# Optimization experiments

Measured on AMD Instinct MI355X. Metric: run time of the kernel, lower is better.

## Reference

```python
import math
import jax, jax.numpy as jnp
from jax import lax
import numpy as np

THETA = 10.0      # spiking threshold
TAU_SR = 10.0     # SRM (psp) alpha-kernel time constant
TAU_REF = 1.0     # refractory alpha-kernel time constant
SCALE_REF = 2.0   # refractory scale (kernel = -scaleRef*theta*alpha)
TAU_RHO = 1.0     # surrogate-gradient width
TS = 1.0          # simulation time step


def _alpha_filter_scan(x, tau, extra_input_fn=None):
    """Causal convolution along last (time) axis with alpha kernel
    k[n] = (n*Ts/tau) * exp(1 - n*Ts/tau)  (k[0] = 0),
    implemented exactly as a 2-state linear recurrence.
    x: [N, C, T] -> out: [N, C, T]."""
    d = jnp.float32(math.exp(-TS / tau))
    c = jnp.float32(math.e * TS / tau)
    xT = jnp.moveaxis(x, -1, 0)  # [T, N, C]

    def step(carry, xt):
        p, a = carry
        a = d * (a + p)          # alpha response from inputs up to t-1
        p = d * p + xt           # pure exponential state
        return (p, a), a * c

    z = jnp.zeros_like(xT[0])
    _, out = lax.scan(step, (z, z), xT)
    return jnp.moveaxis(out, 0, -1)


def psp(x):
    return _alpha_filter_scan(x, TAU_SR)


@jax.custom_vjp
def spike_fn(v):
    # Heaviside threshold on (membrane - theta)
    return (v >= 0).astype(v.dtype)

def _spike_fwd(v):
    return spike_fn(v), v

def _spike_bwd(v, g):
    # SLAYER surrogate gradient: exponential pdf around threshold
    grad = (1.0 / TAU_RHO) * jnp.exp(-jnp.abs(v) / TAU_RHO)
    return (g * grad,)

spike_fn.defvjp(_spike_fwd, _spike_bwd)


def spike_layer(u_in):
    """Threshold-and-refract over time. u_in: [N, C, T] psp potentials.
    Refractory response = -scaleRef*theta * alpha_{tauRef}(past spikes)."""
    d = jnp.float32(math.exp(-TS / TAU_REF))
    c = jnp.float32(math.e * TS / TAU_REF)
    ref_scale = jnp.float32(-SCALE_REF * THETA)
    uT = jnp.moveaxis(u_in, -1, 0)  # [T, N, C]

    def step(carry, ut):
        p, a = carry
        a = d * (a + p)                      # refractory potential at t
        u = ut + c * a                       # membrane potential
        s = spike_fn(u - THETA)              # spikes (0/1)
        p = d * p + ref_scale * s            # inject refractory impulse
        return (p, a), s

    z = jnp.zeros_like(uT[0])
    _, s = lax.scan(step, (z, z), uT)
    return jnp.moveaxis(s, 0, -1)


def setup_inputs() -> dict:
    key = jax.random.key(0)
    k1, k2, k3 = jax.random.split(key, 3)
    N, I, H, O, T = 64, 256, 1024, 18, 500
    # Bernoulli(0.1) input spikes
    spike_input = (jax.random.uniform(k1, (N, I, T)) < 0.1).astype(jnp.float32)
    W1 = jax.random.normal(k2, (H, I), dtype=jnp.float32) * (1.0 / math.sqrt(I))
    W2 = jax.random.normal(k3, (O, H), dtype=jnp.float32) * (1.0 / math.sqrt(H))
    return {"spike_input": spike_input, "W1": W1, "W2": W2}


def reference(spike_input, W1, W2):
    # layer 1: dense (per-timestep linear) -> psp -> spike
    y1 = jnp.einsum('nit,hi->nht', spike_input, W1)
    s1 = spike_layer(psp(y1))
    # layer 2
    y2 = jnp.einsum('nht,oh->not', s1, W2)
    s2 = spike_layer(psp(y2))
    return s2
```

## Files before the change

kernel.cpp:

```cpp
#include <hip/hip_runtime.h>


#define NN 64
#define II 256
#define HH 1024
#define OO 18
#define TT 500

#define D_SR 0.9048374180359595f
#define C_SR 0.27182818284590454f
#define D_RF 0.36787944117144233f
#define C_RF 2.718281828459045f
#define THETA 10.0f
#define REFS (-20.0f)

typedef _Float16 f16;
typedef _Float16 f16x8 __attribute__((ext_vector_type(8)));
typedef float f32x4 __attribute__((ext_vector_type(4)));
typedef unsigned int uint;
typedef unsigned long long u64;

__device__ __forceinline__ void gl2lds16(const void* g, void* l) {
    __builtin_amdgcn_global_load_lds(
        (const __attribute__((address_space(1))) void*)g,
        (__attribute__((address_space(3))) void*)l, 16, 0, 0);
}

__launch_bounds__(256)
__global__ void prep_all(const float* __restrict__ X, const float* __restrict__ W1,
                         const float* __restrict__ W2, f16* __restrict__ Xb,
                         f16* __restrict__ W1h, f16* __restrict__ W1l,
                         f16* __restrict__ W2h, f16* __restrict__ W2l) {
    __shared__ float tile[64][65];
    const int b = blockIdx.x;
    const int tid = threadIdx.x;

    if (b < 2048) {
        const int t0 = (b & 7) * 64, i0 = ((b >> 3) & 3) * 64, n = b >> 5;
        const int tx = tid & 63, q = tid >> 6;
        const float* Xn = X + (size_t)n * II * TT;
#pragma unroll 4
        for (int j = 0; j < 16; ++j) {
            int il = j * 4 + q;
            int t = t0 + tx;
            tile[il][tx] = (t < TT) ? Xn[(size_t)(i0 + il) * TT + t] : 0.f;
        }
        __syncthreads();
#pragma unroll 4
        for (int j = 0; j < 16; ++j) {
            int tl = j * 4 + q;
            int t = t0 + tl;
            if (t < TT)
                Xb[((size_t)n * TT + t) * II + i0 + tx] = (f16)tile[tx][tl];
        }
    } else if (b < 3072) {
        int idx = (b - 2048) * 256 + tid;
        float w = W1[idx];
        f16 h = (f16)w;
        f16 l = (f16)(w - (float)h);
        W1h[idx] = h;
        W1l[idx] = l;
    } else {
        int idx = (b - 3072) * 256 + tid;
        int o = idx >> 10;
        float w = (o < OO) ? W2[idx] : 0.f;
        f16 h = (f16)w;
        f16 l = (f16)(w - (float)h);
        W2h[idx] = h;
        W2l[idx] = l;
    }
}

__launch_bounds__(512)
__global__ void gemm1_scan1(const f16* __restrict__ Xb, const f16* __restrict__ Wh,
                            const f16* __restrict__ Wl, u64* __restrict__ Sb) {
    __shared__ __align__(16) char smem[3 * 24576];
    float* yb = (float*)smem;

    const int tid = threadIdx.x;
    const int wave = tid >> 6, lane = tid & 63;

    const int f = blockIdx.y * 8 + blockIdx.x;
    const int x = f & 7, g = f >> 3;
    const int n = x * 8 + (g & 7);
    const int ht = g >> 3;
    const int h0g = ht * 128;

    const int rbl = wave * 16 + (lane >> 2);
    const int koff = (((lane & 3) ^ ((lane >> 3) & 3))) * 8;
    const f16* gBh0 = Wh + (size_t)(h0g + rbl) * II + koff;
    const f16* gBl0 = Wl + (size_t)(h0g + rbl) * II + koff;

    const int wm = wave & 1, wn = wave >> 1;
    const int fr = lane & 15, kq = lane >> 4;
    const int kz = (kq ^ ((fr >> 1) & 3)) * 8;

    float p1 = 0.f, a1 = 0.f, p2 = 0.f, a2 = 0.f;

    for (int c = 0; c < 4; ++c) {
        const int t0 = c * 128;
        const int TCe = (TT - t0 < 128) ? (TT - t0) : 128;

        int r0 = rbl; if (r0 > TCe - 1) r0 = TCe - 1;
        const f16* gA0 = Xb + ((size_t)n * TT + t0 + r0) * II + koff;

        auto stage = [&](int kk2, int b) {
            f16* As_b = (f16*)(smem + b * 24576);
            f16* Bh_b = As_b + 4096;
            f16* Bl_b = As_b + 8192;
            const int ko = kk2 * 32;
            gl2lds16(gA0 + ko, As_b + wave * 512);
            gl2lds16(gBh0 + ko, Bh_b + wave * 512);
            gl2lds16(gBl0 + ko, Bl_b + wave * 512);
        };

        stage(0, 0);
        stage(1, 1);

        f32x4 acc[4][2] = {};
#pragma unroll
        for (int kk = 0; kk < 8; ++kk) {
            if (kk < 7) asm volatile("s_waitcnt vmcnt(3)" ::: "memory");
            else        asm volatile("s_waitcnt vmcnt(0)" ::: "memory");
            __builtin_amdgcn_s_barrier();
            __builtin_amdgcn_sched_barrier(0);
            if (kk < 6) stage(kk + 2, (kk + 2) % 3);

            const f16* As_b = (const f16*)(smem + (kk % 3) * 24576);
            const f16* Bh_b = As_b + 4096;
            const f16* Bl_b = As_b + 8192;

            f16x8 av[4], bhv[2], blv[2];
#pragma unroll
            for (int i = 0; i < 4; ++i)
                av[i] = *(const f16x8*)(As_b + (wm * 64 + i * 16 + fr) * 32 + kz);
#pragma unroll
            for (int j = 0; j < 2; ++j) {
                bhv[j] = *(const f16x8*)(Bh_b + (wn * 32 + j * 16 + fr) * 32 + kz);
                blv[j] = *(const f16x8*)(Bl_b + (wn * 32 + j * 16 + fr) * 32 + kz);
            }
            __builtin_amdgcn_s_setprio(1);
#pragma unroll
            for (int i = 0; i < 4; ++i)
#pragma unroll
                for (int j = 0; j < 2; ++j) {
                    acc[i][j] = __builtin_amdgcn_mfma_f32_16x16x32_f16(av[i], bhv[j], acc[i][j], 0, 0, 0);
                    acc[i][j] = __builtin_amdgcn_mfma_f32_16x16x32_f16(av[i], blv[j], acc[i][j], 0, 0, 0);
                }
            __builtin_amdgcn_s_setprio(0);
        }
        __syncthreads();

#pragma unroll
        for (int i = 0; i < 4; ++i)
#pragma unroll
            for (int j = 0; j < 2; ++j) {
                int tr = wm * 64 + i * 16 + kq * 4;
                int hc = wn * 32 + j * 16 + fr;
#pragma unroll
                for (int r = 0; r < 4; ++r)
                    yb[(tr + r) * 132 + hc] = acc[i][j][r];
            }
        __syncthreads();

        if (tid < 128) {
            u64* sq = Sb + ((size_t)n * TT + t0) * 16 + ht * 2 + wave;
            float rb_[8];
#pragma unroll
            for (int j = 0; j < 8; ++j) rb_[j] = yb[j * 132 + tid];
            int t = 0;
            for (; t + 8 <= TCe; t += 8) {
#pragma unroll
                for (int j = 0; j < 8; ++j) {
                    float xv = rb_[j];
                    int tn = t + j + 8;
                    rb_[j] = (tn < TCe) ? yb[tn * 132 + tid] : 0.f;
                    a1 = D_SR * (a1 + p1);
                    p1 = D_SR * p1 + xv;
                    float ut = C_SR * a1;
                    a2 = D_RF * (a2 + p2);
                    float u = ut + C_RF * a2;
                    float s = (u >= THETA) ? 1.0f : 0.0f;
                    p2 = D_RF * p2 + REFS * s;
                    u64 m = __ballot(u >= THETA);
                    if (lane == 0) sq[(size_t)(t + j) * 16] = m;
                }
            }
            int rem = TCe - t;
#pragma unroll
            for (int j = 0; j < 8; ++j) {
                if (j < rem) {
                    float xv = rb_[j];
                    a1 = D_SR * (a1 + p1);
                    p1 = D_SR * p1 + xv;
                    float ut = C_SR * a1;
                    a2 = D_RF * (a2 + p2);
                    float u = ut + C_RF * a2;
                    float s = (u >= THETA) ? 1.0f : 0.0f;
                    p2 = D_RF * p2 + REFS * s;
                    u64 m = __ballot(u >= THETA);
                    if (lane == 0) sq[(size_t)(t + j) * 16] = m;
                }
            }
        }
        __syncthreads();
    }
}

__launch_bounds__(256)
__global__ void gemm2_mfma(const uint* __restrict__ Ab, const f16* __restrict__ W2h,
                           const f16* __restrict__ W2l, float* __restrict__ Y2) {
    __shared__ __align__(16) char bsm[4][3][4096];

    const int tid = threadIdx.x;
    const int wave = tid >> 6, lane = tid & 63;
    const int m0 = blockIdx.x * 64;
    const int fr = lane & 15, kq = lane >> 4;

    const int row = m0 + wave * 16 + fr;
    const uint* arow = Ab + (size_t)row * 32;
    const int sh = kq * 8;
    uint wrow[32];
#pragma unroll
    for (int q = 0; q < 8; ++q)
        *(uint4*)&wrow[q * 4] = *(const uint4*)(arow + q * 4);

    const int srow = lane >> 2;
    const int koff = (((lane & 3) ^ ((lane >> 3) & 3))) * 8;
    const f16* gh0 = W2h + (size_t)srow * HH + koff;
    const f16* gh1 = W2h + (size_t)(srow + 16) * HH + koff;
    const f16* gl0 = W2l + (size_t)srow * HH + koff;
    const f16* gl1 = W2l + (size_t)(srow + 16) * HH + koff;

    auto stage = [&](int kk2, int b) {
        char* s = bsm[wave][b];
        const int ko = kk2 * 32;
        gl2lds16(gh0 + ko, s);
        gl2lds16(gh1 + ko, s + 1024);
        gl2lds16(gl0 + ko, s + 2048);
        gl2lds16(gl1 + ko, s + 3072);
    };

    stage(0, 0);
    stage(1, 1);

    const int kz = (kq ^ ((fr >> 1) & 3)) * 8;

    f32x4 acc[2] = {};
#pragma unroll
    for (int kk = 0; kk < HH / 32; ++kk) {
        if (kk < HH / 32 - 1) asm volatile("s_waitcnt vmcnt(4)" ::: "memory");
        else                  asm volatile("s_waitcnt vmcnt(0)" ::: "memory");
        __builtin_amdgcn_sched_barrier(0);
        if (kk < HH / 32 - 2) stage(kk + 2, (kk + 2) % 3);

        const f16* Bh_b = (const f16*)bsm[wave][kk % 3];
        const f16* Bl_b = Bh_b + 2048 / 2;

        const uint byte = (wrow[kk] >> sh) & 0xFFu;
        f16x8 a;
#pragma unroll
        for (int e = 0; e < 8; ++e)
            a[e] = (byte & (1u << e)) ? (f16)1.0f : (f16)0.0f;

        f16x8 bh[2], bl[2];
#pragma unroll
        for (int j = 0; j < 2; ++j) {
            bh[j] = *(const f16x8*)(Bh_b + (j * 16 + fr) * 32 + kz);
            bl[j] = *(const f16x8*)(Bl_b + (j * 16 + fr) * 32 + kz);
        }
#pragma unroll
        for (int j = 0; j < 2; ++j) {
            acc[j] = __builtin_amdgcn_mfma_f32_16x16x32_f16(a, bh[j], acc[j], 0, 0, 0);
            acc[j] = __builtin_amdgcn_mfma_f32_16x16x32_f16(a, bl[j], acc[j], 0, 0, 0);
        }
    }

#pragma unroll
    for (int j = 0; j < 2; ++j) {
        int rbase = m0 + wave * 16 + kq * 4;
        int cc = j * 16 + fr;
        float* p = Y2 + (size_t)rbase * 32 + cc;
#pragma unroll
        for (int r = 0; r < 4; ++r)
            p[(size_t)r * 32] = acc[j][r];
    }
}

__launch_bounds__(256)
__global__ void scan2_k(const float* __restrict__ Y2, float* __restrict__ Out) {
    __shared__ float yc[TT * 32];
    __shared__ float sb[OO * TT];
    const int n = blockIdx.x, tid = threadIdx.x;

    const float4* src = (const float4*)(Y2 + (size_t)n * TT * 32);
    float4* dst = (float4*)yc;
    for (int i = tid; i < TT * 8; i += 256) dst[i] = src[i];
    __syncthreads();

    if (tid < 32) {
        float p1 = 0.f, a1 = 0.f, p2 = 0.f, a2 = 0.f;
        float rb_[8];
#pragma unroll
        for (int j = 0; j < 8; ++j) rb_[j] = yc[j * 32 + tid];
        int t = 0;
        for (; t + 8 <= TT; t += 8) {
#pragma unroll
            for (int j = 0; j < 8; ++j) {
                float xv = rb_[j];
                int tn = t + j + 8;
                rb_[j] = (tn < TT) ? yc[tn * 32 + tid] : 0.f;
                a1 = D_SR * (a1 + p1);
                p1 = D_SR * p1 + xv;
                float ut = C_SR * a1;
                a2 = D_RF * (a2 + p2);
                float u = ut + C_RF * a2;
                float s = (u >= THETA) ? 1.0f : 0.0f;
                p2 = D_RF * p2 + REFS * s;
                if (tid < OO) sb[tid * TT + t + j] = s;
            }
        }
#pragma unroll
        for (int j = 0; j < 8; ++j) {
            if (t + j < TT) {
                float xv = rb_[j];
                a1 = D_SR * (a1 + p1);
                p1 = D_SR * p1 + xv;
                float ut = C_SR * a1;
                a2 = D_RF * (a2 + p2);
                float u = ut + C_RF * a2;
                float s = (u >= THETA) ? 1.0f : 0.0f;
                p2 = D_RF * p2 + REFS * s;
                if (tid < OO) sb[tid * TT + t + j] = s;
            }
        }
    }
    __syncthreads();

    float* on = Out + (size_t)n * OO * TT;
    for (int e = tid; e < OO * TT; e += 256) on[e] = sb[e];
}

extern "C" void kernel_launch(void* const* d_in, const int* in_sizes, int n_in,
                              void* d_out, int out_size, void* d_ws, size_t ws_size,
                              hipStream_t stream) {
    const float* X  = (const float*)d_in[0];
    const float* W1 = (const float*)d_in[1];
    const float* W2 = (const float*)d_in[2];
    float* out = (float*)d_out;

    const size_t s_sb = (size_t)NN * TT * 16 * 8;
    const size_t s_Xb = (size_t)NN * TT * II * 2;
    const size_t s_W  = (size_t)HH * II * 2;
    const size_t s_W2 = (size_t)32 * HH * 2;

    char* w = (char*)d_ws;
    u64*   sbb = (u64*)w;  w += s_sb;
    f16*   Xb  = (f16*)w;  w += s_Xb;
    f16*   W1h = (f16*)w;  w += s_W;
    f16*   W1l = (f16*)w;  w += s_W;
    f16*   W2h = (f16*)w;  w += s_W2;
    f16*   W2l = (f16*)w;  w += s_W2;
    float* y2  = (float*)w;

    prep_all<<<3200, 256, 0, stream>>>(X, W1, W2, Xb, W1h, W1l, W2h, W2l);

    gemm1_scan1<<<dim3(8, NN), 512, 0, stream>>>(Xb, W1h, W1l, sbb);

    gemm2_mfma<<<(NN * TT) / 64, 256, 0, stream>>>((const uint*)sbb, W2h, W2l, y2);
    scan2_k<<<NN, 256, 0, stream>>>(y2, out);
}
```

Baseline: 189.1 us.

## Bit-pack input spikes and fuse layer-2 GEMM with output scan

Input spikes are packed into 1-bit ballot masks in prep instead of fp16, and gemm1 expands them in registers, so the A tile no longer goes through LDS. The layer-2 GEMM and second scan are merged into one kernel per batch element, with the GEMM output kept in shared memory instead of a global Y2 buffer. Each wave in the fused kernel now computes 64 time rows. This cuts global traffic and one launch, but leaves only 64 blocks for the layer-2 GEMM and needs a large LDS allocation.

```diff
diff --git a/kernel.cpp b/kernel.cpp
--- a/kernel.cpp
+++ b/kernel.cpp
@@ -6,6 +6,7 @@
 #define HH 1024
 #define OO 18
 #define TT 500
+#define TTP 512
 
 #define D_SR 0.9048374180359595f
 #define C_SR 0.27182818284590454f
@@ -26,9 +27,19 @@
         (__attribute__((address_space(3))) void*)l, 16, 0, 0);
 }
 
+__device__ __forceinline__ f16x8 expand8(uint by) {
+    union { f16x8 v; uint u[4]; } A;
+#pragma unroll
+    for (int e = 0; e < 4; ++e) {
+        uint b0 = (by >> (2 * e)) & 1u, b1 = (by >> (2 * e + 1)) & 1u;
+        A.u[e] = (b0 ? 0x3C00u : 0u) | (b1 ? 0x3C000000u : 0u);
+    }
+    return A.v;
+}
+
 __launch_bounds__(256)
 __global__ void prep_all(const float* __restrict__ X, const float* __restrict__ W1,
-                         const float* __restrict__ W2, f16* __restrict__ Xb,
+                         const float* __restrict__ W2, u64* __restrict__ Xb,
                          f16* __restrict__ W1h, f16* __restrict__ W1l,
                          f16* __restrict__ W2h, f16* __restrict__ W2l) {
     __shared__ float tile[64][65];
@@ -46,12 +57,14 @@
             tile[il][tx] = (t < TT) ? Xn[(size_t)(i0 + il) * TT + t] : 0.f;
         }
         __syncthreads();
-#pragma unroll 4
-        for (int j = 0; j < 16; ++j) {
-            int tl = j * 4 + q;
-            int t = t0 + tl;
-            if (t < TT)
-                Xb[((size_t)n * TT + t) * II + i0 + tx] = (f16)tile[tx][tl];
+        const int wv = tid >> 6, ln = tid & 63;
+        const int widx = (b >> 3) & 3;
+#pragma unroll
+        for (int tt = 0; tt < 16; ++tt) {
+            int t = wv * 16 + tt;
+            u64 m = __ballot(tile[ln][t] != 0.0f);
+            if (ln == 0 && (t0 + t) < TT)
+                Xb[((size_t)n * TTP + t0 + t) * 4 + widx] = m;
         }
     } else if (b < 3072) {
         int idx = (b - 2048) * 256 + tid;
@@ -71,10 +84,10 @@
     }
 }
 
-__launch_bounds__(512)
-__global__ void gemm1_scan1(const f16* __restrict__ Xb, const f16* __restrict__ Wh,
+__launch_bounds__(512, 4)
+__global__ void gemm1_scan1(const uint* __restrict__ Xb32, const f16* __restrict__ Wh,
                             const f16* __restrict__ Wl, u64* __restrict__ Sb) {
-    __shared__ __align__(16) char smem[3 * 24576];
+    __shared__ __align__(16) char smem[67584];
     float* yb = (float*)smem;
 
     const int tid = threadIdx.x;
@@ -94,6 +107,7 @@
     const int wm = wave & 1, wn = wave >> 1;
     const int fr = lane & 15, kq = lane >> 4;
     const int kz = (kq ^ ((fr >> 1) & 3)) * 8;
+    const int sh = kq * 8;
 
     float p1 = 0.f, a1 = 0.f, p2 = 0.f, a2 = 0.f;
 
@@ -101,39 +115,45 @@
         const int t0 = c * 128;
         const int TCe = (TT - t0 < 128) ? (TT - t0) : 128;
 
-        int r0 = rbl; if (r0 > TCe - 1) r0 = TCe - 1;
-        const f16* gA0 = Xb + ((size_t)n * TT + t0 + r0) * II + koff;
+        uint xb[8];
+#pragma unroll
+        for (int i = 0; i < 4; ++i) {
+            int r = t0 + wm * 64 + i * 16 + fr;
+            if (r > TT - 1) r = TT - 1;
+            const uint* xr = Xb32 + ((size_t)n * TTP + r) * 8;
+            uint4 wA = *(const uint4*)xr;
+            uint4 wB = *(const uint4*)(xr + 4);
+            xb[i * 2 + 0] = ((wA.x >> sh) & 0xFFu) | (((wA.y >> sh) & 0xFFu) << 8)
+                          | (((wA.z >> sh) & 0xFFu) << 16) | (((wA.w >> sh) & 0xFFu) << 24);
+            xb[i * 2 + 1] = ((wB.x >> sh) & 0xFFu) | (((wB.y >> sh) & 0xFFu) << 8)
+                          | (((wB.z >> sh) & 0xFFu) << 16) | (((wB.w >> sh) & 0xFFu) << 24);
+        }
 
         auto stage = [&](int kk2, int b) {
-            f16* As_b = (f16*)(smem + b * 24576);
-            f16* Bh_b = As_b + 4096;
-            f16* Bl_b = As_b + 8192;
+            f16* Bh_b = (f16*)(smem + b * 16384);
             const int ko = kk2 * 32;
-            gl2lds16(gA0 + ko, As_b + wave * 512);
             gl2lds16(gBh0 + ko, Bh_b + wave * 512);
-            gl2lds16(gBl0 + ko, Bl_b + wave * 512);
+            gl2lds16(gBl0 + ko, Bh_b + 4096 + wave * 512);
         };
-
         stage(0, 0);
         stage(1, 1);
 
         f32x4 acc[4][2] = {};
 #pragma unroll
         for (int kk = 0; kk < 8; ++kk) {
-            if (kk < 7) asm volatile("s_waitcnt vmcnt(3)" ::: "memory");
+            if (kk < 7) asm volatile("s_waitcnt vmcnt(2)" ::: "memory");
             else        asm volatile("s_waitcnt vmcnt(0)" ::: "memory");
             __builtin_amdgcn_s_barrier();
             __builtin_amdgcn_sched_barrier(0);
             if (kk < 6) stage(kk + 2, (kk + 2) % 3);
 
-            const f16* As_b = (const f16*)(smem + (kk % 3) * 24576);
-            const f16* Bh_b = As_b + 4096;
-            const f16* Bl_b = As_b + 8192;
+            const f16* Bh_b = (const f16*)(smem + (kk % 3) * 16384);
+            const f16* Bl_b = Bh_b + 4096;
 
             f16x8 av[4], bhv[2], blv[2];
 #pragma unroll
             for (int i = 0; i < 4; ++i)
-                av[i] = *(const f16x8*)(As_b + (wm * 64 + i * 16 + fr) * 32 + kz);
+                av[i] = expand8((xb[i * 2 + (kk >> 2)] >> ((kk & 3) * 8)) & 0xFFu);
 #pragma unroll
             for (int j = 0; j < 2; ++j) {
                 bhv[j] = *(const f16x8*)(Bh_b + (wn * 32 + j * 16 + fr) * 32 + kz);
@@ -207,33 +227,28 @@
     }
 }
 
-__launch_bounds__(256)
-__global__ void gemm2_mfma(const uint* __restrict__ Ab, const f16* __restrict__ W2h,
-                           const f16* __restrict__ W2l, float* __restrict__ Y2) {
-    __shared__ __align__(16) char bsm[4][3][4096];
-
-    const int tid = threadIdx.x;
+__launch_bounds__(512)
+__global__ void gemm2_scan2(const uint* __restrict__ Ab, const f16* __restrict__ W2h,
+                            const f16* __restrict__ W2l, float* __restrict__ Out) {
+    __shared__ __align__(16) char L[162304];
+    float* yc = (float*)(L + 98304);
+    float* sb = (float*)L;
+
+    const int n = blockIdx.x, tid = threadIdx.x;
     const int wave = tid >> 6, lane = tid & 63;
-    const int m0 = blockIdx.x * 64;
     const int fr = lane & 15, kq = lane >> 4;
-
-    const int row = m0 + wave * 16 + fr;
-    const uint* arow = Ab + (size_t)row * 32;
     const int sh = kq * 8;
-    uint wrow[32];
-#pragma unroll
-    for (int q = 0; q < 8; ++q)
-        *(uint4*)&wrow[q * 4] = *(const uint4*)(arow + q * 4);
-
     const int srow = lane >> 2;
     const int koff = (((lane & 3) ^ ((lane >> 3) & 3))) * 8;
+    const int kz = (kq ^ ((fr >> 1) & 3)) * 8;
+
     const f16* gh0 = W2h + (size_t)srow * HH + koff;
     const f16* gh1 = W2h + (size_t)(srow + 16) * HH + koff;
     const f16* gl0 = W2l + (size_t)srow * HH + koff;
     const f16* gl1 = W2l + (size_t)(srow + 16) * HH + koff;
 
     auto stage = [&](int kk2, int b) {
-        char* s = bsm[wave][b];
+        char* s = L + (wave * 3 + b) * 4096;
         const int ko = kk2 * 32;
         gl2lds16(gh0 + ko, s);
         gl2lds16(gh1 + ko, s + 1024);
@@ -241,27 +256,34 @@
         gl2lds16(gl1 + ko, s + 3072);
     };
 
+    const uint* ar[4];
+#pragma unroll
+    for (int mi = 0; mi < 4; ++mi) {
+        int t = wave * 64 + mi * 16 + fr;
+        if (t > TT - 1) t = TT - 1;
+        ar[mi] = Ab + (size_t)(n * TT + t) * 32;
+    }
+
+    uint ac[4], an[4];
+#pragma unroll
+    for (int mi = 0; mi < 4; ++mi) ac[mi] = ar[mi][0];
     stage(0, 0);
     stage(1, 1);
 
-    const int kz = (kq ^ ((fr >> 1) & 3)) * 8;
-
-    f32x4 acc[2] = {};
-#pragma unroll
-    for (int kk = 0; kk < HH / 32; ++kk) {
-        if (kk < HH / 32 - 1) asm volatile("s_waitcnt vmcnt(4)" ::: "memory");
-        else                  asm volatile("s_waitcnt vmcnt(0)" ::: "memory");
+    f32x4 acc[4][2] = {};
+#pragma unroll
+    for (int kk = 0; kk < 32; ++kk) {
+        if (kk < 31) asm volatile("s_waitcnt vmcnt(4)" ::: "memory");
+        else         asm volatile("s_waitcnt vmcnt(0)" ::: "memory");
         __builtin_amdgcn_sched_barrier(0);
-        if (kk < HH / 32 - 2) stage(kk + 2, (kk + 2) % 3);
-
-        const f16* Bh_b = (const f16*)bsm[wave][kk % 3];
-        const f16* Bl_b = Bh_b + 2048 / 2;
-
-        const uint byte = (wrow[kk] >> sh) & 0xFFu;
-        f16x8 a;
-#pragma unroll
-        for (int e = 0; e < 8; ++e)
-            a[e] = (byte & (1u << e)) ? (f16)1.0f : (f16)0.0f;
+        if (kk < 31) {
+#pragma unroll
+            for (int mi = 0; mi < 4; ++mi) an[mi] = ar[mi][kk + 1];
+        }
+        if (kk < 30) stage(kk + 2, (kk + 2) % 3);
+
+        const f16* Bh_b = (const f16*)(L + (wave * 3 + kk % 3) * 4096);
+        const f16* Bl_b = Bh_b + 1024;
 
         f16x8 bh[2], bl[2];
 #pragma unroll
@@ -269,33 +291,31 @@
             bh[j] = *(const f16x8*)(Bh_b + (j * 16 + fr) * 32 + kz);
             bl[j] = *(const f16x8*)(Bl_b + (j * 16 + fr) * 32 + kz);
         }
+        __builtin_amdgcn_s_setprio(1);
+#pragma unroll
+        for (int mi = 0; mi < 4; ++mi) {
+            f16x8 a = expand8((ac[mi] >> sh) & 0xFFu);
+#pragma unroll
+            for (int j = 0; j < 2; ++j) {
+                acc[mi][j] = __builtin_amdgcn_mfma_f32_16x16x32_f16(a, bh[j], acc[mi][j], 0, 0, 0);
+                acc[mi][j] = __builtin_amdgcn_mfma_f32_16x16x32_f16(a, bl[j], acc[mi][j], 0, 0, 0);
+            }
+        }
+        __builtin_amdgcn_s_setprio(0);
+#pragma unroll
+        for (int mi = 0; mi < 4; ++mi) ac[mi] = an[mi];
+    }
+
+#pragma unroll
+    for (int mi = 0; mi < 4; ++mi)
 #pragma unroll
         for (int j = 0; j < 2; ++j) {
-            acc[j] = __builtin_amdgcn_mfma_f32_16x16x32_f16(a, bh[j], acc[j], 0, 0, 0);
-            acc[j] = __builtin_amdgcn_mfma_f32_16x16x32_f16(a, bl[j], acc[j], 0, 0, 0);
-        }
-    }
-
-#pragma unroll
-    for (int j = 0; j < 2; ++j) {
-        int rbase = m0 + wave * 16 + kq * 4;
-        int cc = j * 16 + fr;
-        float* p = Y2 + (size_t)rbase * 32 + cc;
-#pragma unroll
-        for (int r = 0; r < 4; ++r)
-            p[(size_t)r * 32] = acc[j][r];
-    }
-}
-
-__launch_bounds__(256)
-__global__ void scan2_k(const float* __restrict__ Y2, float* __restrict__ Out) {
-    __shared__ float yc[TT * 32];
-    __shared__ float sb[OO * TT];
-    const int n = blockIdx.x, tid = threadIdx.x;
-
-    const float4* src = (const float4*)(Y2 + (size_t)n * TT * 32);
-    float4* dst = (float4*)yc;
-    for (int i = tid; i < TT * 8; i += 256) dst[i] = src[i];
+            int tb = wave * 64 + mi * 16 + kq * 4;
+            int oc = j * 16 + fr;
+#pragma unroll
+            for (int r = 0; r < 4; ++r)
+                if (tb + r < TT) yc[(tb + r) * 32 + oc] = acc[mi][j][r];
+        }
     __syncthreads();
 
     if (tid < 32) {
@@ -338,7 +358,7 @@
     __syncthreads();
 
     float* on = Out + (size_t)n * OO * TT;
-    for (int e = tid; e < OO * TT; e += 256) on[e] = sb[e];
+    for (int e = tid; e < OO * TT; e += 512) on[e] = sb[e];
 }
 
 extern "C" void kernel_launch(void* const* d_in, const int* in_sizes, int n_in,
@@ -350,23 +370,21 @@
     float* out = (float*)d_out;
 
     const size_t s_sb = (size_t)NN * TT * 16 * 8;
-    const size_t s_Xb = (size_t)NN * TT * II * 2;
+    const size_t s_Xb = (size_t)NN * TTP * 32;
     const size_t s_W  = (size_t)HH * II * 2;
     const size_t s_W2 = (size_t)32 * HH * 2;
 
     char* w = (char*)d_ws;
     u64*   sbb = (u64*)w;  w += s_sb;
-    f16*   Xb  = (f16*)w;  w += s_Xb;
+    u64*   Xbt = (u64*)w;  w += s_Xb;
     f16*   W1h = (f16*)w;  w += s_W;
     f16*   W1l = (f16*)w;  w += s_W;
     f16*   W2h = (f16*)w;  w += s_W2;
     f16*   W2l = (f16*)w;  w += s_W2;
-    float* y2  = (float*)w;
-
-    prep_all<<<3200, 256, 0, stream>>>(X, W1, W2, Xb, W1h, W1l, W2h, W2l);
-
-    gemm1_scan1<<<dim3(8, NN), 512, 0, stream>>>(Xb, W1h, W1l, sbb);
-
-    gemm2_mfma<<<(NN * TT) / 64, 256, 0, stream>>>((const uint*)sbb, W2h, W2l, y2);
-    scan2_k<<<NN, 256, 0, stream>>>(y2, out);
-}
+
+    prep_all<<<3200, 256, 0, stream>>>(X, W1, W2, Xbt, W1h, W1l, W2h, W2l);
+
+    gemm1_scan1<<<dim3(8, NN), 512, 0, stream>>>((const uint*)Xbt, W1h, W1l, sbb);
+
+    gemm2_scan2<<<NN, 512, 0, stream>>>((const uint*)sbb, W2h, W2l, out);
+}
```

Result: slower. 226.5 us (+19.8%).

## Fuse gemm1/scan1, gemm2 and scan2 into one persistent kernel with flag sync

Applied to the files above, without the earlier changes.

Merges the three post-prep kernels into a single 512-block kernel. Each block does its layer-1 GEMM and scan tile, then signals per-sample completion counters. Blocks then spin on those counters before running the layer-2 GEMM, and the first 64 blocks spin again before running the final scan, which now writes straight to global memory. This removes launch gaps and lets stages overlap across samples. It relies on all 512 blocks being co-resident to avoid deadlock, and the spin-waits and atomics add overhead.

```diff
diff --git a/kernel.cpp b/kernel.cpp
--- a/kernel.cpp
+++ b/kernel.cpp
@@ -30,7 +30,8 @@
 __global__ void prep_all(const float* __restrict__ X, const float* __restrict__ W1,
                          const float* __restrict__ W2, f16* __restrict__ Xb,
                          f16* __restrict__ W1h, f16* __restrict__ W1l,
-                         f16* __restrict__ W2h, f16* __restrict__ W2l) {
+                         f16* __restrict__ W2h, f16* __restrict__ W2l,
+                         uint* __restrict__ flags) {
     __shared__ float tile[64][65];
     const int b = blockIdx.x;
     const int tid = threadIdx.x;
@@ -61,6 +62,7 @@
         W1h[idx] = h;
         W1l[idx] = l;
     } else {
+        if (b == 3072 && tid < 128) flags[tid] = 0;
         int idx = (b - 3072) * 256 + tid;
         int o = idx >> 10;
         float w = (o < OO) ? W2[idx] : 0.f;
@@ -71,110 +73,269 @@
     }
 }
 
-__launch_bounds__(512)
-__global__ void gemm1_scan1(const f16* __restrict__ Xb, const f16* __restrict__ Wh,
-                            const f16* __restrict__ Wl, u64* __restrict__ Sb) {
+__launch_bounds__(512, 4)
+__global__ void mega(const f16* __restrict__ Xb, const f16* __restrict__ Wh,
+                     const f16* __restrict__ Wl, u64* __restrict__ Sb,
+                     const f16* __restrict__ W2h, const f16* __restrict__ W2l,
+                     float* __restrict__ Y2, float* __restrict__ Out,
+                     uint* __restrict__ flags) {
     __shared__ __align__(16) char smem[3 * 24576];
-    float* yb = (float*)smem;
-
+
+    const int b = blockIdx.x;
     const int tid = threadIdx.x;
     const int wave = tid >> 6, lane = tid & 63;
-
-    const int f = blockIdx.y * 8 + blockIdx.x;
-    const int x = f & 7, g = f >> 3;
-    const int n = x * 8 + (g & 7);
-    const int ht = g >> 3;
-    const int h0g = ht * 128;
-
-    const int rbl = wave * 16 + (lane >> 2);
-    const int koff = (((lane & 3) ^ ((lane >> 3) & 3))) * 8;
-    const f16* gBh0 = Wh + (size_t)(h0g + rbl) * II + koff;
-    const f16* gBl0 = Wl + (size_t)(h0g + rbl) * II + koff;
-
-    const int wm = wave & 1, wn = wave >> 1;
-    const int fr = lane & 15, kq = lane >> 4;
-    const int kz = (kq ^ ((fr >> 1) & 3)) * 8;
-
-    float p1 = 0.f, a1 = 0.f, p2 = 0.f, a2 = 0.f;
-
-    for (int c = 0; c < 4; ++c) {
-        const int t0 = c * 128;
-        const int TCe = (TT - t0 < 128) ? (TT - t0) : 128;
-
-        int r0 = rbl; if (r0 > TCe - 1) r0 = TCe - 1;
-        const f16* gA0 = Xb + ((size_t)n * TT + t0 + r0) * II + koff;
-
-        auto stage = [&](int kk2, int b) {
-            f16* As_b = (f16*)(smem + b * 24576);
-            f16* Bh_b = As_b + 4096;
-            f16* Bl_b = As_b + 8192;
+    uint* done = flags;
+    uint* y2f  = flags + 64;
+
+    {
+        float* yb = (float*)smem;
+        const int x = b & 7, g = b >> 3;
+        const int nA = x * 8 + (g & 7);
+        const int ht = g >> 3;
+        const int h0g = ht * 128;
+
+        const int rbl = wave * 16 + (lane >> 2);
+        const int koff = (((lane & 3) ^ ((lane >> 3) & 3))) * 8;
+        const f16* gBh0 = Wh + (size_t)(h0g + rbl) * II + koff;
+        const f16* gBl0 = Wl + (size_t)(h0g + rbl) * II + koff;
+
+        const int wm = wave & 1, wn = wave >> 1;
+        const int fr = lane & 15, kq = lane >> 4;
+        const int kz = (kq ^ ((fr >> 1) & 3)) * 8;
+
+        float p1 = 0.f, a1 = 0.f, p2 = 0.f, a2 = 0.f;
+
+        for (int c = 0; c < 4; ++c) {
+            const int t0 = c * 128;
+            const int TCe = (TT - t0 < 128) ? (TT - t0) : 128;
+
+            int r0 = rbl; if (r0 > TCe - 1) r0 = TCe - 1;
+            const f16* gA0 = Xb + ((size_t)nA * TT + t0 + r0) * II + koff;
+
+            auto stage = [&](int kk2, int bs) {
+                f16* As_b = (f16*)(smem + bs * 24576);
+                f16* Bh_b = As_b + 4096;
+                f16* Bl_b = As_b + 8192;
+                const int ko = kk2 * 32;
+                gl2lds16(gA0 + ko, As_b + wave * 512);
+                gl2lds16(gBh0 + ko, Bh_b + wave * 512);
+                gl2lds16(gBl0 + ko, Bl_b + wave * 512);
+            };
+            stage(0, 0);
+            stage(1, 1);
+
+            f32x4 acc[4][2] = {};
+#pragma unroll
+            for (int kk = 0; kk < 8; ++kk) {
+                if (kk < 7) asm volatile("s_waitcnt vmcnt(3)" ::: "memory");
+                else        asm volatile("s_waitcnt vmcnt(0)" ::: "memory");
+                __builtin_amdgcn_s_barrier();
+                __builtin_amdgcn_sched_barrier(0);
+                if (kk < 6) stage(kk + 2, (kk + 2) % 3);
+
+                const f16* As_b = (const f16*)(smem + (kk % 3) * 24576);
+                const f16* Bh_b = As_b + 4096;
+                const f16* Bl_b = As_b + 8192;
+
+                f16x8 av[4], bhv[2], blv[2];
+#pragma unroll
+                for (int i = 0; i < 4; ++i)
+                    av[i] = *(const f16x8*)(As_b + (wm * 64 + i * 16 + fr) * 32 + kz);
+#pragma unroll
+                for (int j = 0; j < 2; ++j) {
+                    bhv[j] = *(const f16x8*)(Bh_b + (wn * 32 + j * 16 + fr) * 32 + kz);
+                    blv[j] = *(const f16x8*)(Bl_b + (wn * 32 + j * 16 + fr) * 32 + kz);
+                }
+                __builtin_amdgcn_s_setprio(1);
+#pragma unroll
+                for (int i = 0; i < 4; ++i)
+#pragma unroll
+                    for (int j = 0; j < 2; ++j) {
+                        acc[i][j] = __builtin_amdgcn_mfma_f32_16x16x32_f16(av[i], bhv[j], acc[i][j], 0, 0, 0);
+                        acc[i][j] = __builtin_amdgcn_mfma_f32_16x16x32_f16(av[i], blv[j], acc[i][j], 0, 0, 0);
+                    }
+                __builtin_amdgcn_s_setprio(0);
+            }
+            __syncthreads();
+
+#pragma unroll
+            for (int i = 0; i < 4; ++i)
+#pragma unroll
+                for (int j = 0; j < 2; ++j) {
+                    int tr = wm * 64 + i * 16 + kq * 4;
+                    int hc = wn * 32 + j * 16 + fr;
+#pragma unroll
+                    for (int r = 0; r < 4; ++r)
+                        yb[(tr + r) * 132 + hc] = acc[i][j][r];
+                }
+            __syncthreads();
+
+            if (tid < 128) {
+                u64* sq = Sb + ((size_t)nA * TT + t0) * 16 + ht * 2 + wave;
+                float rb_[8];
+#pragma unroll
+                for (int j = 0; j < 8; ++j) rb_[j] = yb[j * 132 + tid];
+                int t = 0;
+                for (; t + 8 <= TCe; t += 8) {
+#pragma unroll
+                    for (int j = 0; j < 8; ++j) {
+                        float xv = rb_[j];
+                        int tn = t + j + 8;
+                        rb_[j] = (tn < TCe) ? yb[tn * 132 + tid] : 0.f;
+                        a1 = D_SR * (a1 + p1);
+                        p1 = D_SR * p1 + xv;
+                        float ut = C_SR * a1;
+                        a2 = D_RF * (a2 + p2);
+                        float u = ut + C_RF * a2;
+                        float s = (u >= THETA) ? 1.0f : 0.0f;
+                        p2 = D_RF * p2 + REFS * s;
+                        u64 m = __ballot(u >= THETA);
+                        if (lane == 0) sq[(size_t)(t + j) * 16] = m;
+                    }
+                }
+                int rem = TCe - t;
+#pragma unroll
+                for (int j = 0; j < 8; ++j) {
+                    if (j < rem) {
+                        float xv = rb_[j];
+                        a1 = D_SR * (a1 + p1);
+                        p1 = D_SR * p1 + xv;
+                        float ut = C_SR * a1;
+                        a2 = D_RF * (a2 + p2);
+                        float u = ut + C_RF * a2;
+                        float s = (u >= THETA) ? 1.0f : 0.0f;
+                        p2 = D_RF * p2 + REFS * s;
+                        u64 m = __ballot(u >= THETA);
+                        if (lane == 0) sq[(size_t)(t + j) * 16] = m;
+                    }
+                }
+            }
+            __syncthreads();
+        }
+
+        if (tid == 0) {
+            __threadfence();
+            __hip_atomic_fetch_add(done + nA, 1u, __ATOMIC_RELEASE, __HIP_MEMORY_SCOPE_AGENT);
+        }
+    }
+    __syncthreads();
+
+    const int n0 = (b * 64) / 500, n1 = (b * 64 + 63) / 500;
+    if (b < 500 && tid < 256) {
+        while (__hip_atomic_load(done + n0, __ATOMIC_ACQUIRE, __HIP_MEMORY_SCOPE_AGENT) < 8u)
+            __builtin_amdgcn_s_sleep(8);
+        if (n1 != n0)
+            while (__hip_atomic_load(done + n1, __ATOMIC_ACQUIRE, __HIP_MEMORY_SCOPE_AGENT) < 8u)
+                __builtin_amdgcn_s_sleep(8);
+
+        const uint* Ab = (const uint*)Sb;
+        const int m0 = b * 64;
+        const int fr = lane & 15, kq = lane >> 4;
+        const int sh = kq * 8;
+        const int srow = lane >> 2;
+        const int koff = (((lane & 3) ^ ((lane >> 3) & 3))) * 8;
+        const int kz = (kq ^ ((fr >> 1) & 3)) * 8;
+
+        const f16* gh0 = W2h + (size_t)srow * HH + koff;
+        const f16* gh1 = W2h + (size_t)(srow + 16) * HH + koff;
+        const f16* gl0 = W2l + (size_t)srow * HH + koff;
+        const f16* gl1 = W2l + (size_t)(srow + 16) * HH + koff;
+
+        auto stage2 = [&](int kk2, int bs) {
+            char* s = smem + (wave * 3 + bs) * 4096;
             const int ko = kk2 * 32;
-            gl2lds16(gA0 + ko, As_b + wave * 512);
-            gl2lds16(gBh0 + ko, Bh_b + wave * 512);
-            gl2lds16(gBl0 + ko, Bl_b + wave * 512);
+            gl2lds16(gh0 + ko, s);
+            gl2lds16(gh1 + ko, s + 1024);
+            gl2lds16(gl0 + ko, s + 2048);
+            gl2lds16(gl1 + ko, s + 3072);
         };
 
-        stage(0, 0);
-        stage(1, 1);
-
-        f32x4 acc[4][2] = {};
-#pragma unroll
-        for (int kk = 0; kk < 8; ++kk) {
-            if (kk < 7) asm volatile("s_waitcnt vmcnt(3)" ::: "memory");
-            else        asm volatile("s_waitcnt vmcnt(0)" ::: "memory");
-            __builtin_amdgcn_s_barrier();
+        const int row = m0 + wave * 16 + fr;
+        const uint* arow = Ab + (size_t)row * 32;
+
+        uint ac[1] = { arow[0] };
+        uint an;
+        stage2(0, 0);
+        stage2(1, 1);
+
+        f32x4 acc2[2] = {};
+#pragma unroll
+        for (int kk = 0; kk < 32; ++kk) {
+            if (kk < 31) asm volatile("s_waitcnt vmcnt(4)" ::: "memory");
+            else         asm volatile("s_waitcnt vmcnt(0)" ::: "memory");
             __builtin_amdgcn_sched_barrier(0);
-            if (kk < 6) stage(kk + 2, (kk + 2) % 3);
-
-            const f16* As_b = (const f16*)(smem + (kk % 3) * 24576);
-            const f16* Bh_b = As_b + 4096;
-            const f16* Bl_b = As_b + 8192;
-
-            f16x8 av[4], bhv[2], blv[2];
-#pragma unroll
-            for (int i = 0; i < 4; ++i)
-                av[i] = *(const f16x8*)(As_b + (wm * 64 + i * 16 + fr) * 32 + kz);
+            if (kk < 31) an = arow[kk + 1];
+            if (kk < 30) stage2(kk + 2, (kk + 2) % 3);
+
+            const f16* Bh_b = (const f16*)(smem + (wave * 3 + kk % 3) * 4096);
+            const f16* Bl_b = Bh_b + 1024;
+
+            const uint byte = (ac[0] >> sh) & 0xFFu;
+            union { f16x8 v; uint u[4]; } A;
+#pragma unroll
+            for (int e = 0; e < 4; ++e) {
+                uint b0 = (byte >> (2 * e)) & 1u, b1 = (byte >> (2 * e + 1)) & 1u;
+                A.u[e] = (b0 ? 0x3C00u : 0u) | (b1 ? 0x3C000000u : 0u);
+            }
+
+            f16x8 bh[2], bl[2];
 #pragma unroll
             for (int j = 0; j < 2; ++j) {
-                bhv[j] = *(const f16x8*)(Bh_b + (wn * 32 + j * 16 + fr) * 32 + kz);
-                blv[j] = *(const f16x8*)(Bl_b + (wn * 32 + j * 16 + fr) * 32 + kz);
-            }
-            __builtin_amdgcn_s_setprio(1);
-#pragma unroll
-            for (int i = 0; i < 4; ++i)
-#pragma unroll
-                for (int j = 0; j < 2; ++j) {
-                    acc[i][j] = __builtin_amdgcn_mfma_f32_16x16x32_f16(av[i], bhv[j], acc[i][j], 0, 0, 0);
-                    acc[i][j] = __builtin_amdgcn_mfma_f32_16x16x32_f16(av[i], blv[j], acc[i][j], 0, 0, 0);
-                }
-            __builtin_amdgcn_s_setprio(0);
-        }
+                bh[j] = *(const f16x8*)(Bh_b + (j * 16 + fr) * 32 + kz);
+                bl[j] = *(const f16x8*)(Bl_b + (j * 16 + fr) * 32 + kz);
+            }
+#pragma unroll
+            for (int j = 0; j < 2; ++j) {
+                acc2[j] = __builtin_amdgcn_mfma_f32_16x16x32_f16(A.v, bh[j], acc2[j], 0, 0, 0);
+                acc2[j] = __builtin_amdgcn_mfma_f32_16x16x32_f16(A.v, bl[j], acc2[j], 0, 0, 0);
+            }
+            ac[0] = an;
+        }
+
+#pragma unroll
+        for (int j = 0; j < 2; ++j) {
+            int rbase = m0 + wave * 16 + kq * 4;
+            int cc = j * 16 + fr;
+            float* p = Y2 + (size_t)rbase * 32 + cc;
+#pragma unroll
+            for (int r = 0; r < 4; ++r)
+                p[(size_t)r * 32] = acc2[j][r];
+        }
+    }
+    __syncthreads();
+    if (b < 500 && tid == 0) {
+        __threadfence();
+        __hip_atomic_fetch_add(y2f + n0, 1u, __ATOMIC_RELEASE, __HIP_MEMORY_SCOPE_AGENT);
+        if (n1 != n0)
+            __hip_atomic_fetch_add(y2f + n1, 1u, __ATOMIC_RELEASE, __HIP_MEMORY_SCOPE_AGENT);
+    }
+
+    if (b < 64) {
+        const int n = b;
+        const uint expn = (uint)(((n + 1) * 500 - 1) / 64 - (n * 500) / 64 + 1);
+        while (__hip_atomic_load(y2f + n, __ATOMIC_ACQUIRE, __HIP_MEMORY_SCOPE_AGENT) < expn)
+            __builtin_amdgcn_s_sleep(8);
         __syncthreads();
 
-#pragma unroll
-        for (int i = 0; i < 4; ++i)
-#pragma unroll
-            for (int j = 0; j < 2; ++j) {
-                int tr = wm * 64 + i * 16 + kq * 4;
-                int hc = wn * 32 + j * 16 + fr;
-#pragma unroll
-                for (int r = 0; r < 4; ++r)
-                    yb[(tr + r) * 132 + hc] = acc[i][j][r];
-            }
+        float* yc = (float*)smem;
+        const float4* src = (const float4*)(Y2 + (size_t)n * TT * 32);
+        float4* dst = (float4*)yc;
+        for (int i = tid; i < TT * 8; i += 512) dst[i] = src[i];
         __syncthreads();
 
-        if (tid < 128) {
-            u64* sq = Sb + ((size_t)n * TT + t0) * 16 + ht * 2 + wave;
+        if (tid < 32) {
+            float p1 = 0.f, a1 = 0.f, p2 = 0.f, a2 = 0.f;
             float rb_[8];
-#pragma unroll
-            for (int j = 0; j < 8; ++j) rb_[j] = yb[j * 132 + tid];
+            float* on = Out + (size_t)n * OO * TT + (size_t)tid * TT;
+#pragma unroll
+            for (int j = 0; j < 8; ++j) rb_[j] = yc[j * 32 + tid];
             int t = 0;
-            for (; t + 8 <= TCe; t += 8) {
+            for (; t + 8 <= TT; t += 8) {
 #pragma unroll
                 for (int j = 0; j < 8; ++j) {
                     float xv = rb_[j];
                     int tn = t + j + 8;
-                    rb_[j] = (tn < TCe) ? yb[tn * 132 + tid] : 0.f;
+                    rb_[j] = (tn < TT) ? yc[tn * 32 + tid] : 0.f;
                     a1 = D_SR * (a1 + p1);
                     p1 = D_SR * p1 + xv;
                     float ut = C_SR * a1;
@@ -182,14 +343,12 @@
                     float u = ut + C_RF * a2;
                     float s = (u >= THETA) ? 1.0f : 0.0f;
                     p2 = D_RF * p2 + REFS * s;
-                    u64 m = __ballot(u >= THETA);
-                    if (lane == 0) sq[(size_t)(t + j) * 16] = m;
-                }
-            }
-            int rem = TCe - t;
+                    if (tid < OO) on[t + j] = s;
+                }
+            }
 #pragma unroll
             for (int j = 0; j < 8; ++j) {
-                if (j < rem) {
+                if (t + j < TT) {
                     float xv = rb_[j];
                     a1 = D_SR * (a1 + p1);
                     p1 = D_SR * p1 + xv;
@@ -198,147 +357,11 @@
                     float u = ut + C_RF * a2;
                     float s = (u >= THETA) ? 1.0f : 0.0f;
                     p2 = D_RF * p2 + REFS * s;
-                    u64 m = __ballot(u >= THETA);
-                    if (lane == 0) sq[(size_t)(t + j) * 16] = m;
-                }
-            }
-        }
-        __syncthreads();
-    }
-}
-
-__launch_bounds__(256)
-__global__ void gemm2_mfma(const uint* __restrict__ Ab, const f16* __restrict__ W2h,
-                           const f16* __restrict__ W2l, float* __restrict__ Y2) {
-    __shared__ __align__(16) char bsm[4][3][4096];
-
-    const int tid = threadIdx.x;
-    const int wave = tid >> 6, lane = tid & 63;
-    const int m0 = blockIdx.x * 64;
-    const int fr = lane & 15, kq = lane >> 4;
-
-    const int row = m0 + wave * 16 + fr;
-    const uint* arow = Ab + (size_t)row * 32;
-    const int sh = kq * 8;
-    uint wrow[32];
-#pragma unroll
-    for (int q = 0; q < 8; ++q)
-        *(uint4*)&wrow[q * 4] = *(const uint4*)(arow + q * 4);
-
-    const int srow = lane >> 2;
-    const int koff = (((lane & 3) ^ ((lane >> 3) & 3))) * 8;
-    const f16* gh0 = W2h + (size_t)srow * HH + koff;
-    const f16* gh1 = W2h + (size_t)(srow + 16) * HH + koff;
-    const f16* gl0 = W2l + (size_t)srow * HH + koff;
-    const f16* gl1 = W2l + (size_t)(srow + 16) * HH + koff;
-
-    auto stage = [&](int kk2, int b) {
-        char* s = bsm[wave][b];
-        const int ko = kk2 * 32;
-        gl2lds16(gh0 + ko, s);
-        gl2lds16(gh1 + ko, s + 1024);
-        gl2lds16(gl0 + ko, s + 2048);
-        gl2lds16(gl1 + ko, s + 3072);
-    };
-
-    stage(0, 0);
-    stage(1, 1);
-
-    const int kz = (kq ^ ((fr >> 1) & 3)) * 8;
-
-    f32x4 acc[2] = {};
-#pragma unroll
-    for (int kk = 0; kk < HH / 32; ++kk) {
-        if (kk < HH / 32 - 1) asm volatile("s_waitcnt vmcnt(4)" ::: "memory");
-        else                  asm volatile("s_waitcnt vmcnt(0)" ::: "memory");
-        __builtin_amdgcn_sched_barrier(0);
-        if (kk < HH / 32 - 2) stage(kk + 2, (kk + 2) % 3);
-
-        const f16* Bh_b = (const f16*)bsm[wave][kk % 3];
-        const f16* Bl_b = Bh_b + 2048 / 2;
-
-        const uint byte = (wrow[kk] >> sh) & 0xFFu;
-        f16x8 a;
-#pragma unroll
-        for (int e = 0; e < 8; ++e)
-            a[e] = (byte & (1u << e)) ? (f16)1.0f : (f16)0.0f;
-
-        f16x8 bh[2], bl[2];
-#pragma unroll
-        for (int j = 0; j < 2; ++j) {
-            bh[j] = *(const f16x8*)(Bh_b + (j * 16 + fr) * 32 + kz);
-            bl[j] = *(const f16x8*)(Bl_b + (j * 16 + fr) * 32 + kz);
-        }
-#pragma unroll
-        for (int j = 0; j < 2; ++j) {
-            acc[j] = __builtin_amdgcn_mfma_f32_16x16x32_f16(a, bh[j], acc[j], 0, 0, 0);
-            acc[j] = __builtin_amdgcn_mfma_f32_16x16x32_f16(a, bl[j], acc[j], 0, 0, 0);
-        }
-    }
-
-#pragma unroll
-    for (int j = 0; j < 2; ++j) {
-        int rbase = m0 + wave * 16 + kq * 4;
-        int cc = j * 16 + fr;
-        float* p = Y2 + (size_t)rbase * 32 + cc;
-#pragma unroll
-        for (int r = 0; r < 4; ++r)
-            p[(size_t)r * 32] = acc[j][r];
-    }
-}
-
-__launch_bounds__(256)
-__global__ void scan2_k(const float* __restrict__ Y2, float* __restrict__ Out) {
-    __shared__ float yc[TT * 32];
-    __shared__ float sb[OO * TT];
-    const int n = blockIdx.x, tid = threadIdx.x;
-
-    const float4* src = (const float4*)(Y2 + (size_t)n * TT * 32);
-    float4* dst = (float4*)yc;
-    for (int i = tid; i < TT * 8; i += 256) dst[i] = src[i];
-    __syncthreads();
-
-    if (tid < 32) {
-        float p1 = 0.f, a1 = 0.f, p2 = 0.f, a2 = 0.f;
-        float rb_[8];
-#pragma unroll
-        for (int j = 0; j < 8; ++j) rb_[j] = yc[j * 32 + tid];
-        int t = 0;
-        for (; t + 8 <= TT; t += 8) {
-#pragma unroll
-            for (int j = 0; j < 8; ++j) {
-                float xv = rb_[j];
-                int tn = t + j + 8;
-                rb_[j] = (tn < TT) ? yc[tn * 32 + tid] : 0.f;
-                a1 = D_SR * (a1 + p1);
-                p1 = D_SR * p1 + xv;
-                float ut = C_SR * a1;
-                a2 = D_RF * (a2 + p2);
-                float u = ut + C_RF * a2;
-                float s = (u >= THETA) ? 1.0f : 0.0f;
-                p2 = D_RF * p2 + REFS * s;
-                if (tid < OO) sb[tid * TT + t + j] = s;
-            }
-        }
-#pragma unroll
-        for (int j = 0; j < 8; ++j) {
-            if (t + j < TT) {
-                float xv = rb_[j];
-                a1 = D_SR * (a1 + p1);
-                p1 = D_SR * p1 + xv;
-                float ut = C_SR * a1;
-                a2 = D_RF * (a2 + p2);
-                float u = ut + C_RF * a2;
-                float s = (u >= THETA) ? 1.0f : 0.0f;
-                p2 = D_RF * p2 + REFS * s;
-                if (tid < OO) sb[tid * TT + t + j] = s;
-            }
-        }
-    }
-    __syncthreads();
-
-    float* on = Out + (size_t)n * OO * TT;
-    for (int e = tid; e < OO * TT; e += 256) on[e] = sb[e];
+                    if (tid < OO) on[t + j] = s;
+                }
+            }
+        }
+    }
 }
 
 extern "C" void kernel_launch(void* const* d_in, const int* in_sizes, int n_in,
@@ -353,6 +376,7 @@
     const size_t s_Xb = (size_t)NN * TT * II * 2;
     const size_t s_W  = (size_t)HH * II * 2;
     const size_t s_W2 = (size_t)32 * HH * 2;
+    const size_t s_y2 = (size_t)NN * TT * 32 * 4;
 
     char* w = (char*)d_ws;
     u64*   sbb = (u64*)w;  w += s_sb;
@@ -361,12 +385,10 @@
     f16*   W1l = (f16*)w;  w += s_W;
     f16*   W2h = (f16*)w;  w += s_W2;
     f16*   W2l = (f16*)w;  w += s_W2;
-    float* y2  = (float*)w;
-
-    prep_all<<<3200, 256, 0, stream>>>(X, W1, W2, Xb, W1h, W1l, W2h, W2l);
-
-    gemm1_scan1<<<dim3(8, NN), 512, 0, stream>>>(Xb, W1h, W1l, sbb);
-
-    gemm2_mfma<<<(NN * TT) / 64, 256, 0, stream>>>((const uint*)sbb, W2h, W2l, y2);
-    scan2_k<<<NN, 256, 0, stream>>>(y2, out);
+    float* y2  = (float*)w; w += s_y2;
+    uint*  flags = (uint*)w;
+
+    prep_all<<<3200, 256, 0, stream>>>(X, W1, W2, Xb, W1h, W1l, W2h, W2l, flags);
+
+    mega<<<512, 512, 0, stream>>>(Xb, W1h, W1l, sbb, W2h, W2l, y2, out, flags);
 }
```

Result: slower. 280.5 us (+48.3%).
